# Kernel tuning notes

Measured on AMD Instinct MI355X. Metric: run time of the kernel, lower is better.

Reference implementation:

```python
import jax, jax.numpy as jnp
import numpy as np

N = 50000      # nodes
E = 800000     # edges (avg degree 16)
LM = 1024      # lm_dim
H = 128        # hidden_channels
OUT = 64       # out_channels


def setup_inputs() -> dict:
    key = jax.random.key(0)
    ks = jax.random.split(key, 13)
    s = 0.02
    return {
        "x": jax.random.normal(ks[0], (N,), dtype=jnp.float32),
        "x_out": jax.random.normal(ks[1], (N, LM), dtype=jnp.float32),
        "c": jax.random.normal(ks[2], (N,), dtype=jnp.float32),
        "edge_index": jax.random.randint(ks[3], (2, E), 0, N, dtype=jnp.int64),
        "edge_weight": jax.random.uniform(ks[4], (E,), dtype=jnp.float32),
        # weights stored as [in, out]
        "Wa": jax.random.normal(ks[5], (1, LM), dtype=jnp.float32) * s,   # aa_linear (no bias)
        "Wc": jax.random.normal(ks[6], (1, LM), dtype=jnp.float32) * s,   # c_linear (no bias)
        "Wl": jax.random.normal(ks[7], (LM, LM), dtype=jnp.float32) * s,  # lm_linear
        "bl": jax.random.normal(ks[8], (LM,), dtype=jnp.float32) * s,
        "W1": jax.random.normal(ks[9], (LM, H), dtype=jnp.float32) * s,   # conv1
        "b1": jax.random.normal(ks[10], (H,), dtype=jnp.float32) * s,
        "W3": jax.random.normal(ks[11], (H, OUT), dtype=jnp.float32) * s,  # conv3
        "b3": jax.random.normal(ks[12], (OUT,), dtype=jnp.float32) * s,
    }


def gcn_conv(h, src, dst, ew, W, b, n):
    """PyG GCNConv with normalize=True, add_self_loops=True."""
    h = h @ W                                   # [n, out]
    loop = jnp.arange(n, dtype=src.dtype)
    src_f = jnp.concatenate([src, loop])
    dst_f = jnp.concatenate([dst, loop])
    ew_f = jnp.concatenate([ew, jnp.ones((n,), ew.dtype)])
    deg = jax.ops.segment_sum(ew_f, dst_f, num_segments=n)     # in-degree incl. self-loops
    dis = jnp.where(deg > 0, jax.lax.rsqrt(deg), 0.0)          # deg^{-1/2}
    norm = dis[src_f] * ew_f * dis[dst_f]                      # per-edge coefficient
    out = jax.ops.segment_sum(norm[:, None] * h[src_f], dst_f, num_segments=n)
    return out + b


def reference(x, x_out, c, edge_index, edge_weight, Wa, Wc, Wl, bl, W1, b1, W3, b3):
    # (c_linear(c[:,None]) + aa_linear(x[:,None]) + lm_linear(x_out)).relu()
    h = jax.nn.relu(c[:, None] * Wc[0] + x[:, None] * Wa[0] + x_out @ Wl + bl)  # [N, LM]
    src, dst = edge_index[0], edge_index[1]
    h = jax.nn.relu(gcn_conv(h, src, dst, edge_weight, W1, b1, N))              # [N, H]
    return gcn_conv(h, src, dst, edge_weight, W3, b3, N)                        # [N, OUT]
```

## Files before the change

kernel.cpp:

```cpp
#include <hip/hip_runtime.h>
#include <hip/hip_bf16.h>

typedef unsigned short u16;
typedef __attribute__((ext_vector_type(8))) short bf16x8;
typedef __attribute__((ext_vector_type(4))) float f32x4;

constexpr int NN = 50000;
constexpr int NE = 800000;
constexpr int LM = 1024;
constexpr int HC = 128;
constexpr int OC = 64;

constexpr size_t OFF_ROWPTR = 0;
constexpr size_t OFF_CURSOR = 200192;
constexpr size_t OFF_COUNTS = 400384;
constexpr size_t OFF_INCL   = 600576;
constexpr size_t OFF_BSUM   = 800768;
constexpr size_t OFF_BOFF   = 801024;
constexpr size_t OFF_DIS    = 801280;
constexpr size_t OFF_META   = 1001472;
constexpr size_t OFF_WLT    = 7401472;
constexpr size_t OFF_W1T    = 9498624;
constexpr size_t OFF_H      = 9760768;
constexpr size_t OFF_Y1     = 112160768;
constexpr size_t OFF_DEGF   = 124960768;
constexpr size_t OFF_Y3     = 137760768;

__device__ __forceinline__ u16 f2bf(float f) {
    union { float f; unsigned int u; } a; a.f = f;
    unsigned int u = a.u + 0x7FFFu + ((a.u >> 16) & 1u);
    return (u16)(u >> 16);
}
__device__ __forceinline__ float bf2f(u16 v) {
    union { unsigned int u; float f; } a; a.u = ((unsigned int)v) << 16;
    return a.f;
}
__device__ __forceinline__ ushort2 pkbf(float a, float b) {
    union { __hip_bfloat162 h; ushort2 u; } cv;
    cv.h = __float22bfloat162_rn(make_float2(a, b));
    return cv.u;
}
__device__ __forceinline__ void async_copy16(u16* lds, const u16* g) {
    __builtin_amdgcn_global_load_lds(
        (const __attribute__((address_space(1))) void*)g,
        (__attribute__((address_space(3))) void*)lds, 16, 0, 0);
}

__global__ void k_setup(int* __restrict__ counts, float* __restrict__ degf,
                        const float* __restrict__ Wl, u16* __restrict__ WlT,
                        const float* __restrict__ W1, u16* __restrict__ W1T) {
    int b = blockIdx.x, t = threadIdx.x;
    if (b < 196) {
        int i = b * 256 + t;
        if (i < NN) { counts[i] = 0; degf[i] = 0.f; }
    } else if (b < 196 + 1024) {
        __shared__ float sm[32][33];
        int bb = b - 196;
        int n0 = (bb & 31) * 32, k0 = (bb >> 5) * 32;
        int ty = t >> 5, tx = t & 31;
        #pragma unroll
        for (int i = 0; i < 4; i++)
            sm[ty + i * 8][tx] = Wl[(size_t)(k0 + ty + i * 8) * LM + n0 + tx];
        __syncthreads();
        #pragma unroll
        for (int i = 0; i < 4; i++)
            WlT[(size_t)(n0 + ty + i * 8) * LM + k0 + tx] = f2bf(sm[tx][ty + i * 8]);
    } else {
        int idx = (b - 1220) * 256 + t;
        if (idx < HC * LM) {
            int o = idx >> 10, k = idx & 1023;
            W1T[idx] = f2bf(W1[(size_t)k * HC + o]);
        }
    }
}

__global__ void k_count(const int* __restrict__ ei, const float* __restrict__ ew,
                        int* __restrict__ counts, float* __restrict__ degf) {
    int e = blockIdx.x * 256 + threadIdx.x;
    if (e < NE) {
        int d = ei[NE + e];
        atomicAdd(&counts[d], 1);
        atomicAdd(&degf[d], ew[e]);
    }
}
__global__ void k_scan1(const int* __restrict__ counts, int* __restrict__ incl,
                        int* __restrict__ bsum) {
    __shared__ int sm[1024];
    int t = threadIdx.x, idx = blockIdx.x * 1024 + t;
    int v = (idx < NN) ? counts[idx] : 0;
    sm[t] = v; __syncthreads();
    for (int off = 1; off < 1024; off <<= 1) {
        int add = (t >= off) ? sm[t - off] : 0;
        __syncthreads();
        sm[t] += add;
        __syncthreads();
    }
    if (idx < NN) incl[idx] = sm[t];
    if (t == 1023) bsum[blockIdx.x] = sm[t];
}
__global__ void k_scan2(const int* __restrict__ bsum, int* __restrict__ boff, int nb) {
    if (threadIdx.x == 0 && blockIdx.x == 0) {
        int run = 0;
        for (int i = 0; i < nb; i++) { boff[i] = run; run += bsum[i]; }
    }
}
__global__ void k_scan3(const int* __restrict__ incl, const int* __restrict__ counts,
                        const int* __restrict__ boff, const float* __restrict__ degf,
                        int* __restrict__ rowptr, int* __restrict__ cursor,
                        float* __restrict__ dis) {
    int idx = blockIdx.x * 256 + threadIdx.x;
    if (idx < NN) {
        int rp = incl[idx] - counts[idx] + boff[idx >> 10];
        rowptr[idx] = rp;
        cursor[idx] = rp;
        dis[idx] = rsqrtf(1.0f + degf[idx]);
    } else if (idx == NN) {
        rowptr[NN] = NE;
    }
}
__global__ void k_fill(const int* __restrict__ ei, const float* __restrict__ ew,
                       int* __restrict__ cursor, int2* __restrict__ meta) {
    int e = blockIdx.x * 256 + threadIdx.x;
    if (e < NE) {
        int d = ei[NE + e];
        int slot = atomicAdd(&cursor[d], 1);
        meta[slot] = make_int2(ei[e], __float_as_int(ew[e]));
    }
}
__global__ void k_wnorm(int2* __restrict__ meta, const float* __restrict__ dis) {
    int p = blockIdx.x * 256 + threadIdx.x;
    if (p < NE) {
        int2 m = meta[p];
        meta[p].y = __float_as_int(__int_as_float(m.y) * dis[m.x]);
    }
}

template <int MODE>
__global__ __launch_bounds__(256, 2) void k_gemm(
    const void* __restrict__ Aptr, const u16* __restrict__ Bt, u16* __restrict__ Cout,
    int M, int Nn, int K, int nby,
    const float* __restrict__ xv, const float* __restrict__ cv,
    const float* __restrict__ Wa, const float* __restrict__ Wc,
    const float* __restrict__ bl) {
    __shared__ u16 lA[128 * 64];
    __shared__ u16 lB[128 * 64];
    const int tid = threadIdx.x;
    const int lane = tid & 63, wv = tid >> 6;
    const int mtiles = (M + 127) >> 7;
    int bx, by;
    if (nby > 1) {
        int x = blockIdx.x & 7, j = blockIdx.x >> 3;
        bx = (j & ~7) | x;
        by = j & 7;
        if (bx >= mtiles) return;
    } else {
        bx = blockIdx.x; by = 0;
    }
    const int m0 = bx * 128, n0 = by * 128;
    const int wm = (wv >> 1) * 64, wn = (wv & 1) * 64;
    const int fr = lane & 15, qd = lane >> 4;
    const int nt = K >> 6;

    f32x4 acc[4][4] = {};
    const float* A32 = (const float*)Aptr;

    int srl[4], sslot[4]; const float* sbase[4];
    float4 pf[8];
    if constexpr (MODE == 1) {
        #pragma unroll
        for (int i = 0; i < 4; i++) {
            int cidx = i * 256 + tid;
            srl[i] = cidx >> 3; sslot[i] = cidx & 7;
            int k8 = sslot[i] ^ (srl[i] & 7);
            int row = m0 + srl[i]; if (row >= M) row = M - 1;
            sbase[i] = A32 + (size_t)row * K + k8 * 8;
        }
        #pragma unroll
        for (int i = 0; i < 4; i++) {
            pf[2 * i]     = *(const float4*)(sbase[i]);
            pf[2 * i + 1] = *(const float4*)(sbase[i] + 4);
        }
    }

    for (int kt = 0; kt < nt; kt++) {
        const int k0 = kt << 6;
        __syncthreads();
        #pragma unroll
        for (int i = 0; i < 4; i++) {
            int r0 = i * 32 + wv * 8;
            int rl = r0 + (lane >> 3);
            int slot = lane & 7;
            int k8 = slot ^ (rl & 7);
            int col = n0 + rl; if (col >= Nn) col = Nn - 1;
            const u16* g = Bt + (size_t)col * K + k0 + k8 * 8;
            async_copy16(&lB[r0 * 64], g);
        }
        if constexpr (MODE == 2) {
            #pragma unroll
            for (int i = 0; i < 4; i++) {
                int r0 = i * 32 + wv * 8;
                int rl = r0 + (lane >> 3);
                int slot = lane & 7;
                int k8 = slot ^ (rl & 7);
                int row = m0 + rl; if (row >= M) row = M - 1;
                const u16* g = (const u16*)Aptr + (size_t)row * K + k0 + k8 * 8;
                async_copy16(&lA[r0 * 64], g);
            }
        } else {
            #pragma unroll
            for (int i = 0; i < 4; i++) {
                union { ushort2 u2[4]; bf16x8 v; } pk;
                pk.u2[0] = pkbf(pf[2 * i].x, pf[2 * i].y);
                pk.u2[1] = pkbf(pf[2 * i].z, pf[2 * i].w);
                pk.u2[2] = pkbf(pf[2 * i + 1].x, pf[2 * i + 1].y);
                pk.u2[3] = pkbf(pf[2 * i + 1].z, pf[2 * i + 1].w);
                *(bf16x8*)&lA[srl[i] * 64 + sslot[i] * 8] = pk.v;
            }
        }
        __syncthreads();
        if constexpr (MODE == 1) {
            if (kt + 1 < nt) {
                #pragma unroll
                for (int i = 0; i < 4; i++) {
                    pf[2 * i]     = *(const float4*)(sbase[i] + k0 + 64);
                    pf[2 * i + 1] = *(const float4*)(sbase[i] + k0 + 68);
                }
            }
        }
        #pragma unroll
        for (int s = 0; s < 2; s++) {
            const int slot = (s * 4 + qd) ^ (fr & 7);
            bf16x8 af[4], bfm[4];
            #pragma unroll
            for (int mi = 0; mi < 4; mi++)
                af[mi] = *(const bf16x8*)&lA[(wm + mi * 16 + fr) * 64 + slot * 8];
            #pragma unroll
            for (int ni = 0; ni < 4; ni++)
                bfm[ni] = *(const bf16x8*)&lB[(wn + ni * 16 + fr) * 64 + slot * 8];
            #pragma unroll
            for (int mi = 0; mi < 4; mi++)
                #pragma unroll
                for (int ni = 0; ni < 4; ni++)
                    acc[mi][ni] = __builtin_amdgcn_mfma_f32_16x16x32_bf16(
                        af[mi], bfm[ni], acc[mi][ni], 0, 0, 0);
        }
    }

    int jj[4]; float waj[4], wcj[4], blj[4];
    #pragma unroll
    for (int ni = 0; ni < 4; ni++) {
        jj[ni] = n0 + wn + ni * 16 + fr;
        if constexpr (MODE == 1) { waj[ni] = Wa[jj[ni]]; wcj[ni] = Wc[jj[ni]]; blj[ni] = bl[jj[ni]]; }
    }
    #pragma unroll
    for (int mi = 0; mi < 4; mi++) {
        #pragma unroll
        for (int r = 0; r < 4; r++) {
            int row = m0 + wm + mi * 16 + qd * 4 + r;
            if (row < M) {
                float xb = 0.f, cb = 0.f;
                if constexpr (MODE == 1) { xb = xv[row]; cb = cv[row]; }
                #pragma unroll
                for (int ni = 0; ni < 4; ni++) {
                    float v = acc[mi][ni][r];
                    if constexpr (MODE == 1) {
                        v += xb * waj[ni] + cb * wcj[ni] + blj[ni];
                        v = fmaxf(v, 0.f);
                    }
                    Cout[(size_t)row * Nn + jj[ni]] = f2bf(v);
                }
            }
        }
    }
}

__global__ __launch_bounds__(512) void k_agg1g3(
    const u16* __restrict__ y1, const int* __restrict__ rowptr,
    const int2* __restrict__ meta, const float* __restrict__ dis,
    const float* __restrict__ b1, const float* __restrict__ W3,
    u16* __restrict__ y3) {
    __shared__ float hrow[8][HC];
    int wv = threadIdx.x >> 6, lane = threadIdx.x & 63;
    int node = blockIdx.x * 8 + wv;
    if (node >= NN) return;
    float di = dis[node];
    int p0 = rowptr[node], p1 = rowptr[node + 1];
    ushort2 sv = *(const ushort2*)(y1 + (size_t)node * HC + lane * 2);
    float a0 = di * bf2f(sv.x), a1 = di * bf2f(sv.y);
    #pragma unroll 8
    for (int p = p0; p < p1; ++p) {
        int2 m = meta[p];
        float nm = __int_as_float(m.y);
        ushort2 v = *(const ushort2*)(y1 + (size_t)m.x * HC + lane * 2);
        a0 += nm * bf2f(v.x);
        a1 += nm * bf2f(v.y);
    }
    a0 = fmaxf(di * a0 + b1[lane * 2], 0.f);
    a1 = fmaxf(di * a1 + b1[lane * 2 + 1], 0.f);
    hrow[wv][lane * 2] = a0;
    hrow[wv][lane * 2 + 1] = a1;
    float acc = 0.f;
    #pragma unroll 8
    for (int k = 0; k < HC; ++k)
        acc += hrow[wv][k] * W3[(size_t)k * OC + lane];
    y3[(size_t)node * OC + lane] = f2bf(acc);
}

__global__ __launch_bounds__(256) void k_agg3(
    const u16* __restrict__ y3, const int* __restrict__ rowptr,
    const int2* __restrict__ meta, const float* __restrict__ dis,
    const float* __restrict__ b3, float* __restrict__ outp) {
    int node = blockIdx.x * 4 + (threadIdx.x >> 6);
    int lane = threadIdx.x & 63;
    if (node >= NN) return;
    float di = dis[node];
    int p0 = rowptr[node], p1 = rowptr[node + 1];
    float a = di * bf2f(y3[(size_t)node * OC + lane]);
    #pragma unroll 8
    for (int p = p0; p < p1; ++p) {
        int2 m = meta[p];
        a += __int_as_float(m.y) * bf2f(y3[(size_t)m.x * OC + lane]);
    }
    outp[(size_t)node * OC + lane] = di * a + b3[lane];
}

extern "C" void kernel_launch(void* const* d_in, const int* in_sizes, int n_in,
                              void* d_out, int out_size, void* d_ws, size_t ws_size,
                              hipStream_t stream) {
    const float* x    = (const float*)d_in[0];
    const float* xout = (const float*)d_in[1];
    const float* c    = (const float*)d_in[2];
    const int*   ei   = (const int*)d_in[3];
    const float* ew   = (const float*)d_in[4];
    const float* Wa   = (const float*)d_in[5];
    const float* Wc   = (const float*)d_in[6];
    const float* Wl   = (const float*)d_in[7];
    const float* bl   = (const float*)d_in[8];
    const float* W1   = (const float*)d_in[9];
    const float* b1   = (const float*)d_in[10];
    const float* W3   = (const float*)d_in[11];
    const float* b3   = (const float*)d_in[12];
    float* outp = (float*)d_out;

    char* ws = (char*)d_ws;
    int*   rowptr = (int*)(ws + OFF_ROWPTR);
    int*   cursor = (int*)(ws + OFF_CURSOR);
    int*   counts = (int*)(ws + OFF_COUNTS);
    int*   incl   = (int*)(ws + OFF_INCL);
    int*   bsum   = (int*)(ws + OFF_BSUM);
    int*   boff   = (int*)(ws + OFF_BOFF);
    float* dis    = (float*)(ws + OFF_DIS);
    int2*  meta   = (int2*)(ws + OFF_META);
    u16*   WlT    = (u16*)(ws + OFF_WLT);
    u16*   W1T    = (u16*)(ws + OFF_W1T);
    u16*   hbuf   = (u16*)(ws + OFF_H);
    u16*   y1     = (u16*)(ws + OFF_Y1);
    float* degf   = (float*)(ws + OFF_DEGF);
    u16*   y3     = (u16*)(ws + OFF_Y3);

    k_setup<<<1732, 256, 0, stream>>>(counts, degf, Wl, WlT, W1, W1T);
    k_count<<<3125, 256, 0, stream>>>(ei, ew, counts, degf);
    k_scan1<<<49, 1024, 0, stream>>>(counts, incl, bsum);
    k_scan2<<<1, 64, 0, stream>>>(bsum, boff, 49);
    k_scan3<<<196, 256, 0, stream>>>(incl, counts, boff, degf, rowptr, cursor, dis);
    k_fill <<<3125, 256, 0, stream>>>(ei, ew, cursor, meta);
    k_wnorm<<<3125, 256, 0, stream>>>(meta, dis);

    k_gemm<1><<<392 * 8, 256, 0, stream>>>(xout, WlT, hbuf, NN, LM, LM, 8,
                                           x, c, Wa, Wc, bl);
    k_gemm<2><<<391, 256, 0, stream>>>(hbuf, W1T, y1, NN, HC, LM, 1,
                                       nullptr, nullptr, nullptr, nullptr, nullptr);
    k_agg1g3<<<6250, 512, 0, stream>>>(y1, rowptr, meta, dis, b1, W3, y3);
    k_agg3<<<12500, 256, 0, stream>>>(y3, rowptr, meta, dis, b3, outp);
}
```

Baseline: 714.3 us.

## Widen lm GEMM tile to 128x256, shrink conv1 GEMM tile, fold scan2 and wnorm

The big x_out@Wl GEMM now computes a 128x256 output tile per block, so each fp32 A tile is loaded and converted to bf16 once per two B halves, which halves the redundant A traffic and conversion work. The conv1 GEMM uses 64-row tiles to launch twice as many blocks for better occupancy. The block-offset scan kernel is folded into k_scan3 with a wave reduction, and the per-edge weight normalisation is folded into k_fill, removing two launches and one pass over meta. The wider tile doubles accumulator registers, which may reduce occupancy.

```diff
diff --git a/kernel.cpp b/kernel.cpp
--- a/kernel.cpp
+++ b/kernel.cpp
@@ -98,19 +98,19 @@
     if (idx < NN) incl[idx] = sm[t];
     if (t == 1023) bsum[blockIdx.x] = sm[t];
 }
-__global__ void k_scan2(const int* __restrict__ bsum, int* __restrict__ boff, int nb) {
-    if (threadIdx.x == 0 && blockIdx.x == 0) {
-        int run = 0;
-        for (int i = 0; i < nb; i++) { boff[i] = run; run += bsum[i]; }
-    }
-}
 __global__ void k_scan3(const int* __restrict__ incl, const int* __restrict__ counts,
-                        const int* __restrict__ boff, const float* __restrict__ degf,
+                        const int* __restrict__ bsum, const float* __restrict__ degf,
                         int* __restrict__ rowptr, int* __restrict__ cursor,
                         float* __restrict__ dis) {
+    int seg = blockIdx.x >> 2;
+    int lane = threadIdx.x & 63;
+    int v = (lane < seg) ? bsum[lane] : 0;
+    #pragma unroll
+    for (int off = 32; off > 0; off >>= 1) v += __shfl_down(v, off, 64);
+    int boffv = __shfl(v, 0, 64);
     int idx = blockIdx.x * 256 + threadIdx.x;
     if (idx < NN) {
-        int rp = incl[idx] - counts[idx] + boff[idx >> 10];
+        int rp = incl[idx] - counts[idx] + boffv;
         rowptr[idx] = rp;
         cursor[idx] = rp;
         dis[idx] = rsqrtf(1.0f + degf[idx]);
@@ -119,70 +119,142 @@
     }
 }
 __global__ void k_fill(const int* __restrict__ ei, const float* __restrict__ ew,
+                       const float* __restrict__ dis,
                        int* __restrict__ cursor, int2* __restrict__ meta) {
     int e = blockIdx.x * 256 + threadIdx.x;
     if (e < NE) {
+        int s = ei[e];
         int d = ei[NE + e];
         int slot = atomicAdd(&cursor[d], 1);
-        meta[slot] = make_int2(ei[e], __float_as_int(ew[e]));
-    }
-}
-__global__ void k_wnorm(int2* __restrict__ meta, const float* __restrict__ dis) {
-    int p = blockIdx.x * 256 + threadIdx.x;
-    if (p < NE) {
-        int2 m = meta[p];
-        meta[p].y = __float_as_int(__int_as_float(m.y) * dis[m.x]);
-    }
-}
-
-template <int MODE>
-__global__ __launch_bounds__(256, 2) void k_gemm(
-    const void* __restrict__ Aptr, const u16* __restrict__ Bt, u16* __restrict__ Cout,
-    int M, int Nn, int K, int nby,
+        meta[slot] = make_int2(s, __float_as_int(ew[e] * dis[s]));
+    }
+}
+
+__global__ __launch_bounds__(256, 2) void k_gemm1(
+    const float* __restrict__ A32, const u16* __restrict__ Bt, u16* __restrict__ Cout,
     const float* __restrict__ xv, const float* __restrict__ cv,
     const float* __restrict__ Wa, const float* __restrict__ Wc,
     const float* __restrict__ bl) {
     __shared__ u16 lA[128 * 64];
+    __shared__ u16 lB[2][128 * 64];
+    const int tid = threadIdx.x;
+    const int lane = tid & 63, wv = tid >> 6;
+    const int bx = ((blockIdx.x >> 5) << 3) | (blockIdx.x & 7);
+    const int by = (blockIdx.x >> 3) & 3;
+    if (bx >= 391) return;
+    const int m0 = bx * 128, n0 = by * 256;
+    const int wm = (wv >> 1) * 64, wn = (wv & 1) * 64;
+    const int fr = lane & 15, qd = lane >> 4;
+
+    f32x4 acc[2][4][4] = {};
+
+    int srl[4], sslot[4]; const float* sbase[4];
+    float4 pf[8];
+    #pragma unroll
+    for (int i = 0; i < 4; i++) {
+        int cidx = i * 256 + tid;
+        srl[i] = cidx >> 3; sslot[i] = cidx & 7;
+        int k8 = sslot[i] ^ (srl[i] & 7);
+        int row = m0 + srl[i]; if (row >= NN) row = NN - 1;
+        sbase[i] = A32 + (size_t)row * LM + k8 * 8;
+    }
+    #pragma unroll
+    for (int i = 0; i < 4; i++) {
+        pf[2 * i]     = *(const float4*)(sbase[i]);
+        pf[2 * i + 1] = *(const float4*)(sbase[i] + 4);
+    }
+
+    for (int kt = 0; kt < 16; kt++) {
+        const int k0 = kt << 6;
+        __syncthreads();
+        #pragma unroll
+        for (int h = 0; h < 2; h++)
+            #pragma unroll
+            for (int i = 0; i < 4; i++) {
+                int r0 = i * 32 + wv * 8;
+                int rl = r0 + (lane >> 3);
+                int slot = lane & 7;
+                int k8 = slot ^ (rl & 7);
+                const u16* g = Bt + (size_t)(n0 + h * 128 + rl) * LM + k0 + k8 * 8;
+                async_copy16(&lB[h][r0 * 64], g);
+            }
+        #pragma unroll
+        for (int i = 0; i < 4; i++) {
+            union { ushort2 u2[4]; bf16x8 v; } pk;
+            pk.u2[0] = pkbf(pf[2 * i].x, pf[2 * i].y);
+            pk.u2[1] = pkbf(pf[2 * i].z, pf[2 * i].w);
+            pk.u2[2] = pkbf(pf[2 * i + 1].x, pf[2 * i + 1].y);
+            pk.u2[3] = pkbf(pf[2 * i + 1].z, pf[2 * i + 1].w);
+            *(bf16x8*)&lA[srl[i] * 64 + sslot[i] * 8] = pk.v;
+        }
+        __syncthreads();
+        if (kt < 15) {
+            #pragma unroll
+            for (int i = 0; i < 4; i++) {
+                pf[2 * i]     = *(const float4*)(sbase[i] + k0 + 64);
+                pf[2 * i + 1] = *(const float4*)(sbase[i] + k0 + 68);
+            }
+        }
+        #pragma unroll
+        for (int s = 0; s < 2; s++) {
+            const int slot = (s * 4 + qd) ^ (fr & 7);
+            bf16x8 af[4];
+            #pragma unroll
+            for (int mi = 0; mi < 4; mi++)
+                af[mi] = *(const bf16x8*)&lA[(wm + mi * 16 + fr) * 64 + slot * 8];
+            #pragma unroll
+            for (int h = 0; h < 2; h++) {
+                bf16x8 bfm[4];
+                #pragma unroll
+                for (int ni = 0; ni < 4; ni++)
+                    bfm[ni] = *(const bf16x8*)&lB[h][(wn + ni * 16 + fr) * 64 + slot * 8];
+                #pragma unroll
+                for (int mi = 0; mi < 4; mi++)
+                    #pragma unroll
+                    for (int ni = 0; ni < 4; ni++)
+                        acc[h][mi][ni] = __builtin_amdgcn_mfma_f32_16x16x32_bf16(
+                            af[mi], bfm[ni], acc[h][mi][ni], 0, 0, 0);
+            }
+        }
+    }
+
+    #pragma unroll
+    for (int h = 0; h < 2; h++) {
+        int jj[4]; float waj[4], wcj[4], blj[4];
+        #pragma unroll
+        for (int ni = 0; ni < 4; ni++) {
+            jj[ni] = n0 + h * 128 + wn + ni * 16 + fr;
+            waj[ni] = Wa[jj[ni]]; wcj[ni] = Wc[jj[ni]]; blj[ni] = bl[jj[ni]];
+        }
+        #pragma unroll
+        for (int mi = 0; mi < 4; mi++)
+            #pragma unroll
+            for (int r = 0; r < 4; r++) {
+                int row = m0 + wm + mi * 16 + qd * 4 + r;
+                if (row < NN) {
+                    float xb = xv[row], cb = cv[row];
+                    #pragma unroll
+                    for (int ni = 0; ni < 4; ni++) {
+                        float v = acc[h][mi][ni][r] + xb * waj[ni] + cb * wcj[ni] + blj[ni];
+                        Cout[(size_t)row * LM + jj[ni]] = f2bf(fmaxf(v, 0.f));
+                    }
+                }
+            }
+    }
+}
+
+__global__ __launch_bounds__(256) void k_gemm2(
+    const u16* __restrict__ Abf, const u16* __restrict__ Bt, u16* __restrict__ Cout) {
+    __shared__ u16 lA[64 * 64];
     __shared__ u16 lB[128 * 64];
     const int tid = threadIdx.x;
     const int lane = tid & 63, wv = tid >> 6;
-    const int mtiles = (M + 127) >> 7;
-    int bx, by;
-    if (nby > 1) {
-        int x = blockIdx.x & 7, j = blockIdx.x >> 3;
-        bx = (j & ~7) | x;
-        by = j & 7;
-        if (bx >= mtiles) return;
-    } else {
-        bx = blockIdx.x; by = 0;
-    }
-    const int m0 = bx * 128, n0 = by * 128;
-    const int wm = (wv >> 1) * 64, wn = (wv & 1) * 64;
+    const int m0 = blockIdx.x * 64;
+    const int wm = (wv >> 1) * 32, wn = (wv & 1) * 64;
     const int fr = lane & 15, qd = lane >> 4;
-    const int nt = K >> 6;
-
-    f32x4 acc[4][4] = {};
-    const float* A32 = (const float*)Aptr;
-
-    int srl[4], sslot[4]; const float* sbase[4];
-    float4 pf[8];
-    if constexpr (MODE == 1) {
-        #pragma unroll
-        for (int i = 0; i < 4; i++) {
-            int cidx = i * 256 + tid;
-            srl[i] = cidx >> 3; sslot[i] = cidx & 7;
-            int k8 = sslot[i] ^ (srl[i] & 7);
-            int row = m0 + srl[i]; if (row >= M) row = M - 1;
-            sbase[i] = A32 + (size_t)row * K + k8 * 8;
-        }
-        #pragma unroll
-        for (int i = 0; i < 4; i++) {
-            pf[2 * i]     = *(const float4*)(sbase[i]);
-            pf[2 * i + 1] = *(const float4*)(sbase[i] + 4);
-        }
-    }
-
-    for (int kt = 0; kt < nt; kt++) {
+    f32x4 acc[2][4] = {};
+
+    for (int kt = 0; kt < 16; kt++) {
         const int k0 = kt << 6;
         __syncthreads();
         #pragma unroll
@@ -191,87 +263,49 @@
             int rl = r0 + (lane >> 3);
             int slot = lane & 7;
             int k8 = slot ^ (rl & 7);
-            int col = n0 + rl; if (col >= Nn) col = Nn - 1;
-            const u16* g = Bt + (size_t)col * K + k0 + k8 * 8;
+            const u16* g = Bt + (size_t)rl * LM + k0 + k8 * 8;
             async_copy16(&lB[r0 * 64], g);
         }
-        if constexpr (MODE == 2) {
-            #pragma unroll
-            for (int i = 0; i < 4; i++) {
-                int r0 = i * 32 + wv * 8;
-                int rl = r0 + (lane >> 3);
-                int slot = lane & 7;
-                int k8 = slot ^ (rl & 7);
-                int row = m0 + rl; if (row >= M) row = M - 1;
-                const u16* g = (const u16*)Aptr + (size_t)row * K + k0 + k8 * 8;
-                async_copy16(&lA[r0 * 64], g);
-            }
-        } else {
-            #pragma unroll
-            for (int i = 0; i < 4; i++) {
-                union { ushort2 u2[4]; bf16x8 v; } pk;
-                pk.u2[0] = pkbf(pf[2 * i].x, pf[2 * i].y);
-                pk.u2[1] = pkbf(pf[2 * i].z, pf[2 * i].w);
-                pk.u2[2] = pkbf(pf[2 * i + 1].x, pf[2 * i + 1].y);
-                pk.u2[3] = pkbf(pf[2 * i + 1].z, pf[2 * i + 1].w);
-                *(bf16x8*)&lA[srl[i] * 64 + sslot[i] * 8] = pk.v;
-            }
-        }
-        __syncthreads();
-        if constexpr (MODE == 1) {
-            if (kt + 1 < nt) {
-                #pragma unroll
-                for (int i = 0; i < 4; i++) {
-                    pf[2 * i]     = *(const float4*)(sbase[i] + k0 + 64);
-                    pf[2 * i + 1] = *(const float4*)(sbase[i] + k0 + 68);
-                }
-            }
-        }
+        #pragma unroll
+        for (int i = 0; i < 2; i++) {
+            int r0 = i * 32 + wv * 8;
+            int rl = r0 + (lane >> 3);
+            int slot = lane & 7;
+            int k8 = slot ^ (rl & 7);
+            int row = m0 + rl; if (row >= NN) row = NN - 1;
+            const u16* g = Abf + (size_t)row * LM + k0 + k8 * 8;
+            async_copy16(&lA[r0 * 64], g);
+        }
+        __syncthreads();
         #pragma unroll
         for (int s = 0; s < 2; s++) {
             const int slot = (s * 4 + qd) ^ (fr & 7);
-            bf16x8 af[4], bfm[4];
-            #pragma unroll
-            for (int mi = 0; mi < 4; mi++)
+            bf16x8 af[2], bfm[4];
+            #pragma unroll
+            for (int mi = 0; mi < 2; mi++)
                 af[mi] = *(const bf16x8*)&lA[(wm + mi * 16 + fr) * 64 + slot * 8];
             #pragma unroll
             for (int ni = 0; ni < 4; ni++)
                 bfm[ni] = *(const bf16x8*)&lB[(wn + ni * 16 + fr) * 64 + slot * 8];
             #pragma unroll
-            for (int mi = 0; mi < 4; mi++)
+            for (int mi = 0; mi < 2; mi++)
                 #pragma unroll
                 for (int ni = 0; ni < 4; ni++)
                     acc[mi][ni] = __builtin_amdgcn_mfma_f32_16x16x32_bf16(
                         af[mi], bfm[ni], acc[mi][ni], 0, 0, 0);
         }
     }
-
-    int jj[4]; float waj[4], wcj[4], blj[4];
     #pragma unroll
-    for (int ni = 0; ni < 4; ni++) {
-        jj[ni] = n0 + wn + ni * 16 + fr;
-        if constexpr (MODE == 1) { waj[ni] = Wa[jj[ni]]; wcj[ni] = Wc[jj[ni]]; blj[ni] = bl[jj[ni]]; }
-    }
-    #pragma unroll
-    for (int mi = 0; mi < 4; mi++) {
+    for (int mi = 0; mi < 2; mi++)
         #pragma unroll
         for (int r = 0; r < 4; r++) {
             int row = m0 + wm + mi * 16 + qd * 4 + r;
-            if (row < M) {
-                float xb = 0.f, cb = 0.f;
-                if constexpr (MODE == 1) { xb = xv[row]; cb = cv[row]; }
+            if (row < NN) {
                 #pragma unroll
-                for (int ni = 0; ni < 4; ni++) {
-                    float v = acc[mi][ni][r];
-                    if constexpr (MODE == 1) {
-                        v += xb * waj[ni] + cb * wcj[ni] + blj[ni];
-                        v = fmaxf(v, 0.f);
-                    }
-                    Cout[(size_t)row * Nn + jj[ni]] = f2bf(v);
-                }
+                for (int ni = 0; ni < 4; ni++)
+                    Cout[(size_t)row * HC + wn + ni * 16 + fr] = f2bf(acc[mi][ni][r]);
             }
         }
-    }
 }
 
 __global__ __launch_bounds__(512) void k_agg1g3(
@@ -348,7 +382,6 @@
     int*   counts = (int*)(ws + OFF_COUNTS);
     int*   incl   = (int*)(ws + OFF_INCL);
     int*   bsum   = (int*)(ws + OFF_BSUM);
-    int*   boff   = (int*)(ws + OFF_BOFF);
     float* dis    = (float*)(ws + OFF_DIS);
     int2*  meta   = (int2*)(ws + OFF_META);
     u16*   WlT    = (u16*)(ws + OFF_WLT);
@@ -361,15 +394,11 @@
     k_setup<<<1732, 256, 0, stream>>>(counts, degf, Wl, WlT, W1, W1T);
     k_count<<<3125, 256, 0, stream>>>(ei, ew, counts, degf);
     k_scan1<<<49, 1024, 0, stream>>>(counts, incl, bsum);
-    k_scan2<<<1, 64, 0, stream>>>(bsum, boff, 49);
-    k_scan3<<<196, 256, 0, stream>>>(incl, counts, boff, degf, rowptr, cursor, dis);
-    k_fill <<<3125, 256, 0, stream>>>(ei, ew, cursor, meta);
-    k_wnorm<<<3125, 256, 0, stream>>>(meta, dis);
-
-    k_gemm<1><<<392 * 8, 256, 0, stream>>>(xout, WlT, hbuf, NN, LM, LM, 8,
-                                           x, c, Wa, Wc, bl);
-    k_gemm<2><<<391, 256, 0, stream>>>(hbuf, W1T, y1, NN, HC, LM, 1,
-                                       nullptr, nullptr, nullptr, nullptr, nullptr);
+    k_scan3<<<196, 256, 0, stream>>>(incl, counts, bsum, degf, rowptr, cursor, dis);
+    k_fill <<<3125, 256, 0, stream>>>(ei, ew, dis, cursor, meta);
+
+    k_gemm1<<<49 * 32, 256, 0, stream>>>(xout, WlT, hbuf, x, c, Wa, Wc, bl);
+    k_gemm2<<<782, 256, 0, stream>>>(hbuf, W1T, y1);
     k_agg1g3<<<6250, 512, 0, stream>>>(y1, rowptr, meta, dis, b1, W3, y3);
     k_agg3<<<12500, 256, 0, stream>>>(y3, rowptr, meta, dis, b3, outp);
 }
```

New measurement: 707.6 us. Within noise of the previous version (-0.9%).
